# Kernel tuning notes

Hardware: AMD Instinct MI355X
Metric: run time of the kernel (lower is better)

The kernel has to match this reference:

```python
import jax, jax.numpy as jnp
import numpy as np

T, B, I, H, L = 512, 256, 128, 256, 2

def _gru_layer(x, W_ih, W_hh, b_ih, b_hh):
    # x: [T, B, in], W_ih: [3H, in], W_hh: [3H, H], biases: [3H]
    # PyTorch gate order: r, z, n
    Hd = W_hh.shape[1]
    gi = jnp.einsum('tbi,gi->tbg', x, W_ih) + b_ih  # precompute input gates [T,B,3H]

    def step(h, gi_t):
        gh = h @ W_hh.T + b_hh
        i_r, i_z, i_n = jnp.split(gi_t, 3, axis=-1)
        h_r, h_z, h_n = jnp.split(gh, 3, axis=-1)
        r = jax.nn.sigmoid(i_r + h_r)
        z = jax.nn.sigmoid(i_z + h_z)
        n = jnp.tanh(i_n + r * h_n)
        h_new = (1.0 - z) * n + z * h
        return h_new, h_new

    h0 = jnp.zeros((x.shape[1], Hd), dtype=x.dtype)
    _, hs = jax.lax.scan(step, h0, gi)
    return hs  # [T, B, H]

def setup_inputs() -> dict:
    key = jax.random.key(0)
    ks = jax.random.split(key, 11)
    s = 1.0 / np.sqrt(H)
    u = lambda k, shp: jax.random.uniform(k, shp, jnp.float32, -s, s)
    return {
        'x': jax.random.normal(ks[0], (T, B, I), jnp.float32),
        'W_ih0': u(ks[1], (3 * H, I)),
        'W_hh0': u(ks[2], (3 * H, H)),
        'b_ih0': u(ks[3], (3 * H,)),
        'b_hh0': u(ks[4], (3 * H,)),
        'W_ih1': u(ks[5], (3 * H, H)),
        'W_hh1': u(ks[6], (3 * H, H)),
        'b_ih1': u(ks[7], (3 * H,)),
        'b_hh1': u(ks[8], (3 * H,)),
        'W_fc': u(ks[9], (H, H)),
        'b_fc': u(ks[10], (H,)),
    }

def reference(x, W_ih0, W_hh0, b_ih0, b_hh0, W_ih1, W_hh1, b_ih1, b_hh1, W_fc, b_fc):
    h1 = _gru_layer(x, W_ih0, W_hh0, b_ih0, b_hh0)   # [T,B,H]
    h2 = _gru_layer(h1, W_ih1, W_hh1, b_ih1, b_hh1)  # [T,B,H]
    last = h2[-1]                                    # [B,H] last timestep
    return last @ W_fc.T + b_fc
```

## Files before the change

kernel.cpp:

```cpp
#include <hip/hip_runtime.h>

#define TT 512
#define BB 256
#define II 128
#define HH 256
#define LDH 264

typedef __attribute__((ext_vector_type(8))) short short8;
typedef __attribute__((ext_vector_type(4))) float floatx4;
typedef __attribute__((ext_vector_type(4))) float fvec4;
typedef unsigned long long u64;

#define OFF_WIH0 0
#define OFF_WHH0 (OFF_WIH0 + 3 * HH * II)
#define OFF_WIH1 (OFF_WHH0 + 3 * HH * HH)
#define OFF_WHH1 (OFF_WIH1 + 3 * HH * HH)
#define W_TOTAL (OFF_WHH1 + 3 * HH * HH)
#define H1G_OFF W_TOTAL
#define H2G_OFF (H1G_OFF + 2 * BB * HH)
#define WS_SHORTS (H2G_OFF + 2 * BB * HH)
#define FLAGS_OFF_BYTES (WS_SHORTS * 2)
#define FLAG_STRIDE 32

__device__ __forceinline__ short f2bf(float f) {
  unsigned u = __builtin_bit_cast(unsigned, f);
  u = u + 0x7fffu + ((u >> 16) & 1u);
  return (short)(u >> 16);
}
__device__ __forceinline__ float fast_sigmoid(float x) {
  return __fdividef(1.0f, 1.0f + __expf(-x));
}
__device__ __forceinline__ float fast_tanh(float x) {
  return 1.0f - __fdividef(2.0f, 1.0f + __expf(2.0f * x));
}
__device__ __forceinline__ short8 cvt8(const float* __restrict__ p) {
  fvec4 lo = *(const fvec4*)p;
  fvec4 hi = *(const fvec4*)(p + 4);
  short8 r;
  r[0] = f2bf(lo[0]); r[1] = f2bf(lo[1]); r[2] = f2bf(lo[2]); r[3] = f2bf(lo[3]);
  r[4] = f2bf(hi[0]); r[5] = f2bf(hi[1]); r[6] = f2bf(hi[2]); r[7] = f2bf(hi[3]);
  return r;
}
__device__ __forceinline__ u64 ld_sc1(const u64* p) {
  return __hip_atomic_load(p, __ATOMIC_RELAXED, __HIP_MEMORY_SCOPE_AGENT);
}
__device__ __forceinline__ unsigned ld_flag(const unsigned* p) {
  return __hip_atomic_load(p, __ATOMIC_RELAXED, __HIP_MEMORY_SCOPE_AGENT);
}
__device__ __forceinline__ void st_flag(unsigned* p, unsigned v) {
  __hip_atomic_store(p, v, __ATOMIC_RELAXED, __HIP_MEMORY_SCOPE_AGENT);
}

__global__ __launch_bounds__(256) void cvt_weights(
    const float* __restrict__ w0, const float* __restrict__ w1,
    const float* __restrict__ w2, const float* __restrict__ w3,
    short* __restrict__ out) {
  int i = blockIdx.x * 256 + threadIdx.x;
  if (i >= W_TOTAL) return;
  float v;
  if (i < OFF_WHH0)      v = w0[i - OFF_WIH0];
  else if (i < OFF_WIH1) v = w1[i - OFF_WHH0];
  else if (i < OFF_WHH1) v = w2[i - OFF_WIH1];
  else                   v = w3[i - OFF_WHH1];
  out[i] = f2bf(v);
}

__global__ __launch_bounds__(256) void init_state(unsigned* __restrict__ hz,
                                                  unsigned* __restrict__ flags) {
  int i = blockIdx.x * 256 + threadIdx.x;
  if (i < 2 * BB * HH) hz[i] = 0u;
  if (i < 16 * FLAG_STRIDE) flags[i] = 0u;
}

__global__ __launch_bounds__(384) void gru_sync(
    const float* __restrict__ x, const short* __restrict__ wb,
    const float* __restrict__ bih0, const float* __restrict__ bhh0,
    const float* __restrict__ bih1, const float* __restrict__ bhh1,
    const float* __restrict__ Wfc, const float* __restrict__ bfc,
    short* __restrict__ h1g, short* __restrict__ h2g,
    unsigned* __restrict__ flags, float* __restrict__ out) {
  const int tid = threadIdx.x;
  const int lane = tid & 63;
  const int w = tid >> 6;
  const int quad = lane >> 4;
  const int col = lane & 15;
  const int bt = blockIdx.x & 15;
  const int ht = blockIdx.x >> 4;
  const int layer = w / 3, gate = w % 3;
  const int j = ht * 16 + col;

  __shared__ __align__(16) short ldsA[2][16][LDH];
  __shared__ __align__(16) float gt[2][6][16][20];

  const short* wih = wb + (layer ? OFF_WIH1 : OFF_WIH0);
  const short* whh = wb + (layer ? OFF_WHH1 : OFF_WHH0);
  short8 wfI[8], wfH[8];
  if (layer == 0) {
#pragma unroll
    for (int f = 0; f < 4; ++f)
      wfI[f] = *(const short8*)(wih + (gate * HH + j) * II + f * 32 + quad * 8);
#pragma unroll
    for (int f = 4; f < 8; ++f) wfI[f] = short8{0, 0, 0, 0, 0, 0, 0, 0};
  } else {
#pragma unroll
    for (int f = 0; f < 8; ++f)
      wfI[f] = *(const short8*)(wih + (gate * HH + j) * HH + f * 32 + quad * 8);
  }
#pragma unroll
  for (int f = 0; f < 8; ++f)
    wfH[f] = *(const short8*)(whh + (gate * HH + j) * HH + f * 32 + quad * 8);

  const float* bihL = layer ? bih1 : bih0;
  const float* bhhL = layer ? bhh1 : bhh0;
  float bI, bH;
  if (gate == 2) { bI = bihL[2 * HH + j]; bH = bhhL[2 * HH + j]; }
  else { bI = bihL[gate * HH + j] + bhhL[gate * HH + j]; bH = 0.f; }

  float h1a = 0.f, h1b = 0.f, h2a = 0.f, h2b = 0.f;
  const int r1 = tid >> 3, c1 = (tid & 7) * 2;
  const int r2 = (tid - 256) >> 3, c2 = ((tid - 256) & 7) * 2;

  unsigned* fl = flags + bt * FLAG_STRIDE;
  const size_t tbase = (size_t)(bt * 16) * HH;

  for (int p = 0; p <= TT; ++p) {
    short8 ax[4];
    if (w < 3 && p < TT) {
      const float* xr = x + ((size_t)p * BB + bt * 16 + col) * II + quad * 8;
#pragma unroll
      for (int f = 0; f < 4; ++f) ax[f] = cvt8(xr + f * 32);
    }

    if (p > 0) {
      if (tid < 64) {
        const unsigned tgt = (unsigned)p;
        int guard = 0;
        for (;;) {
          unsigned v = tgt;
          if (lane < 16) v = ld_flag(fl + lane);
          if (__all(v >= tgt) || ++guard > (1 << 20)) break;
        }
      }
      __syncthreads();
    }

    {
      const u64* s1 = (const u64*)(h1g + ((p + 1) & 1) * BB * HH + tbase);
      const u64* s2 = (const u64*)(h2g + (p & 1) * BB * HH + tbase);
      u64 t1[4], t2[4];
      if (tid < 256) {
#pragma unroll
        for (int qq = 0; qq < 4; ++qq) t1[qq] = ld_sc1(s1 + tid * 4 + qq);
      }
      if (tid >= 128) {
        const int ti = tid - 128;
#pragma unroll
        for (int qq = 0; qq < 4; ++qq) t2[qq] = ld_sc1(s2 + ti * 4 + qq);
      }
      u64* d1 = (u64*)&ldsA[0][0][0];
      u64* d2 = (u64*)&ldsA[1][0][0];
      if (tid < 256) {
#pragma unroll
        for (int qq = 0; qq < 4; ++qq) {
          int i = tid * 4 + qq, row = i >> 6, c = i & 63;
          d1[row * (LDH / 4) + c] = t1[qq];
        }
      }
      if (tid >= 128) {
        const int ti = tid - 128;
#pragma unroll
        for (int qq = 0; qq < 4; ++qq) {
          int i = ti * 4 + qq, row = i >> 6, c = i & 63;
          d2[row * (LDH / 4) + c] = t2[qq];
        }
      }
    }
    __syncthreads();

    floatx4 aI = floatx4{bI, bI, bI, bI};
    floatx4 aH = floatx4{bH, bH, bH, bH};
    const short* a1 = &ldsA[0][col][0];
    const short* a2 = &ldsA[1][col][0];
    if (layer == 0) {
      if (p < TT) {
#pragma unroll
        for (int f = 0; f < 4; ++f)
          aI = __builtin_amdgcn_mfma_f32_16x16x32_bf16(ax[f], wfI[f], aI, 0, 0, 0);
      }
#pragma unroll
      for (int f = 0; f < 8; ++f) {
        short8 a = *(const short8*)(a1 + f * 32 + quad * 8);
        aH = __builtin_amdgcn_mfma_f32_16x16x32_bf16(a, wfH[f], aH, 0, 0, 0);
      }
    } else {
#pragma unroll
      for (int f = 0; f < 8; ++f) {
        short8 a = *(const short8*)(a1 + f * 32 + quad * 8);
        aI = __builtin_amdgcn_mfma_f32_16x16x32_bf16(a, wfI[f], aI, 0, 0, 0);
      }
#pragma unroll
      for (int f = 0; f < 8; ++f) {
        short8 a = *(const short8*)(a2 + f * 32 + quad * 8);
        aH = __builtin_amdgcn_mfma_f32_16x16x32_bf16(a, wfH[f], aH, 0, 0, 0);
      }
    }
#pragma unroll
    for (int i = 0; i < 4; ++i) {
      gt[0][w][quad * 4 + i][col] = aI[i];
      gt[1][w][quad * 4 + i][col] = aH[i];
    }
    __syncthreads();

    if (tid < 128 && p < TT) {
      float rA = fast_sigmoid(gt[0][0][r1][c1] + gt[1][0][r1][c1]);
      float zA = fast_sigmoid(gt[0][1][r1][c1] + gt[1][1][r1][c1]);
      float nA = fast_tanh(gt[0][2][r1][c1] + rA * gt[1][2][r1][c1]);
      h1a = nA + zA * (h1a - nA);
      float rB = fast_sigmoid(gt[0][0][r1][c1 + 1] + gt[1][0][r1][c1 + 1]);
      float zB = fast_sigmoid(gt[0][1][r1][c1 + 1] + gt[1][1][r1][c1 + 1]);
      float nB = fast_tanh(gt[0][2][r1][c1 + 1] + rB * gt[1][2][r1][c1 + 1]);
      h1b = nB + zB * (h1b - nB);
      unsigned val = ((unsigned)(unsigned short)f2bf(h1b) << 16) |
                     (unsigned)(unsigned short)f2bf(h1a);
      unsigned* dst = (unsigned*)(h1g + (p & 1) * BB * HH +
                                  (bt * 16 + r1) * HH + ht * 16 + c1);
      __hip_atomic_store(dst, val, __ATOMIC_RELAXED, __HIP_MEMORY_SCOPE_AGENT);
    }
    if (tid >= 256 && p > 0) {
      float rA = fast_sigmoid(gt[0][3][r2][c2] + gt[1][3][r2][c2]);
      float zA = fast_sigmoid(gt[0][4][r2][c2] + gt[1][4][r2][c2]);
      float nA = fast_tanh(gt[0][5][r2][c2] + rA * gt[1][5][r2][c2]);
      h2a = nA + zA * (h2a - nA);
      float rB = fast_sigmoid(gt[0][3][r2][c2 + 1] + gt[1][3][r2][c2 + 1]);
      float zB = fast_sigmoid(gt[0][4][r2][c2 + 1] + gt[1][4][r2][c2 + 1]);
      float nB = fast_tanh(gt[0][5][r2][c2 + 1] + rB * gt[1][5][r2][c2 + 1]);
      h2b = nB + zB * (h2b - nB);
      unsigned val = ((unsigned)(unsigned short)f2bf(h2b) << 16) |
                     (unsigned)(unsigned short)f2bf(h2a);
      unsigned* dst = (unsigned*)(h2g + ((p + 1) & 1) * BB * HH +
                                  (bt * 16 + r2) * HH + ht * 16 + c2);
      __hip_atomic_store(dst, val, __ATOMIC_RELAXED, __HIP_MEMORY_SCOPE_AGENT);
    }
    __syncthreads();
    if (tid == 0) st_flag(fl + ht, (unsigned)(p + 1));
  }

  if (tid < 64) {
    const unsigned tgt = (unsigned)(TT + 1);
    int guard = 0;
    for (;;) {
      unsigned v = tgt;
      if (lane < 16) v = ld_flag(fl + lane);
      if (__all(v >= tgt) || ++guard > (1 << 20)) break;
    }
  }
  __syncthreads();
  {
    const u64* s1 = (const u64*)(h2g + 1 * BB * HH + tbase);
    u64 t1[4];
    if (tid < 256) {
#pragma unroll
      for (int qq = 0; qq < 4; ++qq) t1[qq] = ld_sc1(s1 + tid * 4 + qq);
    }
    u64* d1 = (u64*)&ldsA[0][0][0];
    if (tid < 256) {
#pragma unroll
      for (int qq = 0; qq < 4; ++qq) {
        int i = tid * 4 + qq, row = i >> 6, c = i & 63;
        d1[row * (LDH / 4) + c] = t1[qq];
      }
    }
  }
  __syncthreads();
  if (w == 0) {
    float bbv = bfc[j];
    floatx4 acc = floatx4{bbv, bbv, bbv, bbv};
#pragma unroll
    for (int f = 0; f < 8; ++f) {
      short8 a = *(const short8*)(&ldsA[0][col][0] + f * 32 + quad * 8);
      short8 bfrag = cvt8(Wfc + j * HH + f * 32 + quad * 8);
      acc = __builtin_amdgcn_mfma_f32_16x16x32_bf16(a, bfrag, acc, 0, 0, 0);
    }
#pragma unroll
    for (int i = 0; i < 4; ++i)
      out[(size_t)(bt * 16 + quad * 4 + i) * HH + j] = acc[i];
  }
}

extern "C" void kernel_launch(void* const* d_in, const int* in_sizes, int n_in,
                              void* d_out, int out_size, void* d_ws,
                              size_t ws_size, hipStream_t stream) {
  const float* x = (const float*)d_in[0];
  const float* Wih0 = (const float*)d_in[1];
  const float* Whh0 = (const float*)d_in[2];
  const float* bih0 = (const float*)d_in[3];
  const float* bhh0 = (const float*)d_in[4];
  const float* Wih1 = (const float*)d_in[5];
  const float* Whh1 = (const float*)d_in[6];
  const float* bih1 = (const float*)d_in[7];
  const float* bhh1 = (const float*)d_in[8];
  const float* Wfc = (const float*)d_in[9];
  const float* bfc = (const float*)d_in[10];

  short* wb = (short*)d_ws;
  short* h1g = wb + H1G_OFF;
  short* h2g = wb + H2G_OFF;
  unsigned* flags = (unsigned*)((char*)d_ws + FLAGS_OFF_BYTES);
  unsigned* hz = (unsigned*)(wb + H1G_OFF);

  cvt_weights<<<(W_TOTAL + 255) / 256, 256, 0, stream>>>(Wih0, Whh0, Wih1, Whh1, wb);
  init_state<<<(2 * BB * HH + 255) / 256, 256, 0, stream>>>(hz, flags);
  gru_sync<<<256, 384, 0, stream>>>(x, wb, bih0, bhh0, bih1, bhh1, Wfc, bfc,
                                    h1g, h2g, flags, (float*)d_out);
}
```

Baseline: 1.758 ms.

## Interleave four batch groups per block to hide inter-block flag latency

```diff
diff --git a/kernel.cpp b/kernel.cpp
--- a/kernel.cpp
+++ b/kernel.cpp
@@ -84,13 +84,13 @@
   const int w = tid >> 6;
   const int quad = lane >> 4;
   const int col = lane & 15;
-  const int bt = blockIdx.x & 15;
-  const int ht = blockIdx.x >> 4;
+  const int q = blockIdx.x & 3;
+  const int ht = blockIdx.x >> 2;
   const int layer = w / 3, gate = w % 3;
   const int j = ht * 16 + col;
 
-  __shared__ __align__(16) short ldsA[2][16][LDH];
-  __shared__ __align__(16) float gt[2][6][16][20];
+  __shared__ __align__(16) short ldsA[4][2][16][LDH];
+  __shared__ __align__(16) float gt[4][2][6][16][20];
 
   const short* wih = wb + (layer ? OFF_WIH1 : OFF_WIH0);
   const short* whh = wb + (layer ? OFF_WHH1 : OFF_WHH0);
@@ -116,23 +116,21 @@
   if (gate == 2) { bI = bihL[2 * HH + j]; bH = bhhL[2 * HH + j]; }
   else { bI = bihL[gate * HH + j] + bhhL[gate * HH + j]; bH = 0.f; }
 
-  float h1a = 0.f, h1b = 0.f, h2a = 0.f, h2b = 0.f;
   const int r1 = tid >> 3, c1 = (tid & 7) * 2;
   const int r2 = (tid - 256) >> 3, c2 = ((tid - 256) & 7) * 2;
 
-  unsigned* fl = flags + bt * FLAG_STRIDE;
-  const size_t tbase = (size_t)(bt * 16) * HH;
-
-  for (int p = 0; p <= TT; ++p) {
-    short8 ax[4];
-    if (w < 3 && p < TT) {
-      const float* xr = x + ((size_t)p * BB + bt * 16 + col) * II + quad * 8;
-#pragma unroll
-      for (int f = 0; f < 4; ++f) ax[f] = cvt8(xr + f * 32);
-    }
+  float h1aA = 0.f, h1bA = 0.f, h2aA = 0.f, h2bA = 0.f;
+  float h1aB = 0.f, h1bB = 0.f, h2aB = 0.f, h2bB = 0.f;
+  float h1aC = 0.f, h1bC = 0.f, h2aC = 0.f, h2bC = 0.f;
+  float h1aD = 0.f, h1bD = 0.f, h2aD = 0.f, h2bD = 0.f;
+
+  auto slot = [&](int g, int p, short8 (&ax)[4], float& h1a, float& h1b,
+                  float& h2a, float& h2b) {
+    unsigned* fl = flags + (q + 4 * g) * FLAG_STRIDE;
+    const size_t tbase = (size_t)((q + 4 * g) * 16) * HH;
 
     if (p > 0) {
-      if (tid < 64) {
+      if (w == 3) {
         const unsigned tgt = (unsigned)p;
         int guard = 0;
         for (;;) {
@@ -157,8 +155,8 @@
 #pragma unroll
         for (int qq = 0; qq < 4; ++qq) t2[qq] = ld_sc1(s2 + ti * 4 + qq);
       }
-      u64* d1 = (u64*)&ldsA[0][0][0];
-      u64* d2 = (u64*)&ldsA[1][0][0];
+      u64* d1 = (u64*)&ldsA[g][0][0][0];
+      u64* d2 = (u64*)&ldsA[g][1][0][0];
       if (tid < 256) {
 #pragma unroll
         for (int qq = 0; qq < 4; ++qq) {
@@ -179,8 +177,8 @@
 
     floatx4 aI = floatx4{bI, bI, bI, bI};
     floatx4 aH = floatx4{bH, bH, bH, bH};
-    const short* a1 = &ldsA[0][col][0];
-    const short* a2 = &ldsA[1][col][0];
+    const short* a1 = &ldsA[g][0][col][0];
+    const short* a2 = &ldsA[g][1][col][0];
     if (layer == 0) {
       if (p < TT) {
 #pragma unroll
@@ -206,64 +204,81 @@
     }
 #pragma unroll
     for (int i = 0; i < 4; ++i) {
-      gt[0][w][quad * 4 + i][col] = aI[i];
-      gt[1][w][quad * 4 + i][col] = aH[i];
+      gt[g][0][w][quad * 4 + i][col] = aI[i];
+      gt[g][1][w][quad * 4 + i][col] = aH[i];
     }
     __syncthreads();
 
     if (tid < 128 && p < TT) {
-      float rA = fast_sigmoid(gt[0][0][r1][c1] + gt[1][0][r1][c1]);
-      float zA = fast_sigmoid(gt[0][1][r1][c1] + gt[1][1][r1][c1]);
-      float nA = fast_tanh(gt[0][2][r1][c1] + rA * gt[1][2][r1][c1]);
+      float rA = fast_sigmoid(gt[g][0][0][r1][c1] + gt[g][1][0][r1][c1]);
+      float zA = fast_sigmoid(gt[g][0][1][r1][c1] + gt[g][1][1][r1][c1]);
+      float nA = fast_tanh(gt[g][0][2][r1][c1] + rA * gt[g][1][2][r1][c1]);
       h1a = nA + zA * (h1a - nA);
-      float rB = fast_sigmoid(gt[0][0][r1][c1 + 1] + gt[1][0][r1][c1 + 1]);
-      float zB = fast_sigmoid(gt[0][1][r1][c1 + 1] + gt[1][1][r1][c1 + 1]);
-      float nB = fast_tanh(gt[0][2][r1][c1 + 1] + rB * gt[1][2][r1][c1 + 1]);
+      float rB = fast_sigmoid(gt[g][0][0][r1][c1 + 1] + gt[g][1][0][r1][c1 + 1]);
+      float zB = fast_sigmoid(gt[g][0][1][r1][c1 + 1] + gt[g][1][1][r1][c1 + 1]);
+      float nB = fast_tanh(gt[g][0][2][r1][c1 + 1] + rB * gt[g][1][2][r1][c1 + 1]);
       h1b = nB + zB * (h1b - nB);
       unsigned val = ((unsigned)(unsigned short)f2bf(h1b) << 16) |
                      (unsigned)(unsigned short)f2bf(h1a);
       unsigned* dst = (unsigned*)(h1g + (p & 1) * BB * HH +
-                                  (bt * 16 + r1) * HH + ht * 16 + c1);
+                                  ((q + 4 * g) * 16 + r1) * HH + ht * 16 + c1);
       __hip_atomic_store(dst, val, __ATOMIC_RELAXED, __HIP_MEMORY_SCOPE_AGENT);
     }
     if (tid >= 256 && p > 0) {
-      float rA = fast_sigmoid(gt[0][3][r2][c2] + gt[1][3][r2][c2]);
-      float zA = fast_sigmoid(gt[0][4][r2][c2] + gt[1][4][r2][c2]);
-      float nA = fast_tanh(gt[0][5][r2][c2] + rA * gt[1][5][r2][c2]);
+      float rA = fast_sigmoid(gt[g][0][3][r2][c2] + gt[g][1][3][r2][c2]);
+      float zA = fast_sigmoid(gt[g][0][4][r2][c2] + gt[g][1][4][r2][c2]);
+      float nA = fast_tanh(gt[g][0][5][r2][c2] + rA * gt[g][1][5][r2][c2]);
       h2a = nA + zA * (h2a - nA);
-      float rB = fast_sigmoid(gt[0][3][r2][c2 + 1] + gt[1][3][r2][c2 + 1]);
-      float zB = fast_sigmoid(gt[0][4][r2][c2 + 1] + gt[1][4][r2][c2 + 1]);
-      float nB = fast_tanh(gt[0][5][r2][c2 + 1] + rB * gt[1][5][r2][c2 + 1]);
+      float rB = fast_sigmoid(gt[g][0][3][r2][c2 + 1] + gt[g][1][3][r2][c2 + 1]);
+      float zB = fast_sigmoid(gt[g][0][4][r2][c2 + 1] + gt[g][1][4][r2][c2 + 1]);
+      float nB = fast_tanh(gt[g][0][5][r2][c2 + 1] + rB * gt[g][1][5][r2][c2 + 1]);
       h2b = nB + zB * (h2b - nB);
       unsigned val = ((unsigned)(unsigned short)f2bf(h2b) << 16) |
                      (unsigned)(unsigned short)f2bf(h2a);
       unsigned* dst = (unsigned*)(h2g + ((p + 1) & 1) * BB * HH +
-                                  (bt * 16 + r2) * HH + ht * 16 + c2);
+                                  ((q + 4 * g) * 16 + r2) * HH + ht * 16 + c2);
       __hip_atomic_store(dst, val, __ATOMIC_RELAXED, __HIP_MEMORY_SCOPE_AGENT);
     }
     __syncthreads();
     if (tid == 0) st_flag(fl + ht, (unsigned)(p + 1));
-  }
-
-  if (tid < 64) {
+  };
+
+  for (int p = 0; p <= TT; ++p) {
+    short8 axA[4], axB[4], axC[4], axD[4];
+    if (w < 3 && p < TT) {
+      const float* xr = x + ((size_t)p * BB + q * 16 + col) * II + quad * 8;
+#pragma unroll
+      for (int f = 0; f < 4; ++f) {
+        axA[f] = cvt8(xr + f * 32);
+        axB[f] = cvt8(xr + 64 * II + f * 32);
+        axC[f] = cvt8(xr + 128 * II + f * 32);
+        axD[f] = cvt8(xr + 192 * II + f * 32);
+      }
+    }
+    slot(0, p, axA, h1aA, h1bA, h2aA, h2bA);
+    slot(1, p, axB, h1aB, h1bB, h2aB, h2bB);
+    slot(2, p, axC, h1aC, h1bC, h2aC, h2bC);
+    slot(3, p, axD, h1aD, h1bD, h2aD, h2bD);
+  }
+
+  if (w == 3) {
     const unsigned tgt = (unsigned)(TT + 1);
     int guard = 0;
     for (;;) {
-      unsigned v = tgt;
-      if (lane < 16) v = ld_flag(fl + lane);
+      unsigned v = ld_flag(flags + (q + 4 * (lane >> 4)) * FLAG_STRIDE + (lane & 15));
       if (__all(v >= tgt) || ++guard > (1 << 20)) break;
     }
   }
   __syncthreads();
-  {
-    const u64* s1 = (const u64*)(h2g + 1 * BB * HH + tbase);
-    u64 t1[4];
-    if (tid < 256) {
+  if (tid < 256) {
+#pragma unroll
+    for (int g = 0; g < 4; ++g) {
+      const size_t tb = (size_t)((q + 4 * g) * 16) * HH;
+      const u64* s1 = (const u64*)(h2g + 1 * BB * HH + tb);
+      u64 t1[4];
 #pragma unroll
       for (int qq = 0; qq < 4; ++qq) t1[qq] = ld_sc1(s1 + tid * 4 + qq);
-    }
-    u64* d1 = (u64*)&ldsA[0][0][0];
-    if (tid < 256) {
+      u64* d1 = (u64*)&ldsA[g][0][0][0];
 #pragma unroll
       for (int qq = 0; qq < 4; ++qq) {
         int i = tid * 4 + qq, row = i >> 6, c = i & 63;
@@ -272,18 +287,19 @@
     }
   }
   __syncthreads();
-  if (w == 0) {
+  if (w < 4) {
+    const int g = w;
     float bbv = bfc[j];
     floatx4 acc = floatx4{bbv, bbv, bbv, bbv};
 #pragma unroll
     for (int f = 0; f < 8; ++f) {
-      short8 a = *(const short8*)(&ldsA[0][col][0] + f * 32 + quad * 8);
+      short8 a = *(const short8*)(&ldsA[g][0][col][0] + f * 32 + quad * 8);
       short8 bfrag = cvt8(Wfc + j * HH + f * 32 + quad * 8);
       acc = __builtin_amdgcn_mfma_f32_16x16x32_bf16(a, bfrag, acc, 0, 0, 0);
     }
 #pragma unroll
     for (int i = 0; i < 4; ++i)
-      out[(size_t)(bt * 16 + quad * 4 + i) * HH + j] = acc[i];
+      out[(size_t)((q + 4 * g) * 16 + quad * 4 + i) * HH + j] = acc[i];
   }
 }
 
@@ -310,6 +326,6 @@
 
   cvt_weights<<<(W_TOTAL + 255) / 256, 256, 0, stream>>>(Wih0, Whh0, Wih1, Whh1, wb);
   init_state<<<(2 * BB * HH + 255) / 256, 256, 0, stream>>>(hz, flags);
-  gru_sync<<<256, 384, 0, stream>>>(x, wb, bih0, bhh0, bih1, bhh1, Wfc, bfc,
-                                    h1g, h2g, flags, (float*)d_out);
-}
+  gru_sync<<<64, 384, 0, stream>>>(x, wb, bih0, bhh0, bih1, bhh1, Wfc, bfc,
+                                   h1g, h2g, flags, (float*)d_out);
+}
```

After: 6.339 ms. 261% more time.

## Replace flag barriers with step-tagged hidden-state words for per-element synchronization

Applied to the files above, without the earlier changes.

```diff
diff --git a/kernel.cpp b/kernel.cpp
--- a/kernel.cpp
+++ b/kernel.cpp
@@ -16,11 +16,10 @@
 #define OFF_WIH1 (OFF_WHH0 + 3 * HH * HH)
 #define OFF_WHH1 (OFF_WIH1 + 3 * HH * HH)
 #define W_TOTAL (OFF_WHH1 + 3 * HH * HH)
-#define H1G_OFF W_TOTAL
-#define H2G_OFF (H1G_OFF + 2 * BB * HH)
-#define WS_SHORTS (H2G_OFF + 2 * BB * HH)
-#define FLAGS_OFF_BYTES (WS_SHORTS * 2)
-#define FLAG_STRIDE 32
+#define HPAR (BB * (HH / 2))
+#define HT_WORDS (2 * HPAR)
+#define H1T_OFF_BYTES (W_TOTAL * 2)
+#define H2T_OFF_BYTES (H1T_OFF_BYTES + HT_WORDS * 8)
 
 __device__ __forceinline__ short f2bf(float f) {
   unsigned u = __builtin_bit_cast(unsigned, f);
@@ -44,10 +43,7 @@
 __device__ __forceinline__ u64 ld_sc1(const u64* p) {
   return __hip_atomic_load(p, __ATOMIC_RELAXED, __HIP_MEMORY_SCOPE_AGENT);
 }
-__device__ __forceinline__ unsigned ld_flag(const unsigned* p) {
-  return __hip_atomic_load(p, __ATOMIC_RELAXED, __HIP_MEMORY_SCOPE_AGENT);
-}
-__device__ __forceinline__ void st_flag(unsigned* p, unsigned v) {
+__device__ __forceinline__ void st_sc1(u64* p, u64 v) {
   __hip_atomic_store(p, v, __ATOMIC_RELAXED, __HIP_MEMORY_SCOPE_AGENT);
 }
 
@@ -65,11 +61,13 @@
   out[i] = f2bf(v);
 }
 
-__global__ __launch_bounds__(256) void init_state(unsigned* __restrict__ hz,
-                                                  unsigned* __restrict__ flags) {
+__global__ __launch_bounds__(256) void init_state(u64* __restrict__ h1t,
+                                                  u64* __restrict__ h2t) {
   int i = blockIdx.x * 256 + threadIdx.x;
-  if (i < 2 * BB * HH) hz[i] = 0u;
-  if (i < 16 * FLAG_STRIDE) flags[i] = 0u;
+  if (i < HT_WORDS) {
+    h1t[i] = 0ull;
+    h2t[i] = (1ull << 32);
+  }
 }
 
 __global__ __launch_bounds__(384) void gru_sync(
@@ -77,8 +75,7 @@
     const float* __restrict__ bih0, const float* __restrict__ bhh0,
     const float* __restrict__ bih1, const float* __restrict__ bhh1,
     const float* __restrict__ Wfc, const float* __restrict__ bfc,
-    short* __restrict__ h1g, short* __restrict__ h2g,
-    unsigned* __restrict__ flags, float* __restrict__ out) {
+    u64* __restrict__ h1t, u64* __restrict__ h2t, float* __restrict__ out) {
   const int tid = threadIdx.x;
   const int lane = tid & 63;
   const int w = tid >> 6;
@@ -88,6 +85,7 @@
   const int ht = blockIdx.x >> 4;
   const int layer = w / 3, gate = w % 3;
   const int j = ht * 16 + col;
+  (void)lane;
 
   __shared__ __align__(16) short ldsA[2][16][LDH];
   __shared__ __align__(16) float gt[2][6][16][20];
@@ -118,10 +116,10 @@
 
   float h1a = 0.f, h1b = 0.f, h2a = 0.f, h2b = 0.f;
   const int r1 = tid >> 3, c1 = (tid & 7) * 2;
-  const int r2 = (tid - 256) >> 3, c2 = ((tid - 256) & 7) * 2;
-
-  unsigned* fl = flags + bt * FLAG_STRIDE;
-  const size_t tbase = (size_t)(bt * 16) * HH;
+  const int r2 = (tid - 256) >> 3;
+  const int c2 = ((tid - 256) & 7) * 2;
+
+  const int tilebase = bt * 16 * (HH / 2);
 
   for (int p = 0; p <= TT; ++p) {
     short8 ax[4];
@@ -131,47 +129,48 @@
       for (int f = 0; f < 4; ++f) ax[f] = cvt8(xr + f * 32);
     }
 
-    if (p > 0) {
-      if (tid < 64) {
-        const unsigned tgt = (unsigned)p;
-        int guard = 0;
-        for (;;) {
-          unsigned v = tgt;
-          if (lane < 16) v = ld_flag(fl + lane);
-          if (__all(v >= tgt) || ++guard > (1 << 20)) break;
+    u64 w1[8], w2[8];
+    {
+      const u64* s1w = h1t + ((p + 1) & 1) * HPAR + tilebase;
+      const u64* s2w = h2t + (p & 1) * HPAR + tilebase;
+      const unsigned tg = (unsigned)p;
+      int guard = 0;
+      for (;;) {
+        bool ok = true;
+        if (tid < 256) {
+#pragma unroll
+          for (int k = 0; k < 8; ++k) w1[k] = ld_sc1(s1w + tid * 8 + k);
+#pragma unroll
+          for (int k = 0; k < 8; ++k) ok &= ((unsigned)(w1[k] >> 32) == tg);
         }
-      }
-      __syncthreads();
-    }
-
+        if (tid >= 128) {
+          const int ti = tid - 128;
+#pragma unroll
+          for (int k = 0; k < 8; ++k) w2[k] = ld_sc1(s2w + ti * 8 + k);
+#pragma unroll
+          for (int k = 0; k < 8; ++k) ok &= ((unsigned)(w2[k] >> 32) == tg);
+        }
+        if (p == 0 || __all(ok) || ++guard > (1 << 16)) break;
+      }
+    }
     {
-      const u64* s1 = (const u64*)(h1g + ((p + 1) & 1) * BB * HH + tbase);
-      const u64* s2 = (const u64*)(h2g + (p & 1) * BB * HH + tbase);
-      u64 t1[4], t2[4];
-      if (tid < 256) {
-#pragma unroll
-        for (int qq = 0; qq < 4; ++qq) t1[qq] = ld_sc1(s1 + tid * 4 + qq);
-      }
-      if (tid >= 128) {
-        const int ti = tid - 128;
-#pragma unroll
-        for (int qq = 0; qq < 4; ++qq) t2[qq] = ld_sc1(s2 + ti * 4 + qq);
-      }
       u64* d1 = (u64*)&ldsA[0][0][0];
       u64* d2 = (u64*)&ldsA[1][0][0];
       if (tid < 256) {
 #pragma unroll
         for (int qq = 0; qq < 4; ++qq) {
+          u64 v = (w1[2 * qq] & 0xffffffffull) | (w1[2 * qq + 1] << 32);
           int i = tid * 4 + qq, row = i >> 6, c = i & 63;
-          d1[row * (LDH / 4) + c] = t1[qq];
+          d1[row * (LDH / 4) + c] = v;
         }
       }
       if (tid >= 128) {
         const int ti = tid - 128;
 #pragma unroll
         for (int qq = 0; qq < 4; ++qq) {
+          u64 v = (w2[2 * qq] & 0xffffffffull) | (w2[2 * qq + 1] << 32);
           int i = ti * 4 + qq, row = i >> 6, c = i & 63;
-          d2[row * (LDH / 4) + c] = t2[qq];
+          d2[row * (LDH / 4) + c] = v;
         }
       }
     }
@@ -222,9 +221,9 @@
       h1b = nB + zB * (h1b - nB);
       unsigned val = ((unsigned)(unsigned short)f2bf(h1b) << 16) |
                      (unsigned)(unsigned short)f2bf(h1a);
-      unsigned* dst = (unsigned*)(h1g + (p & 1) * BB * HH +
-                                  (bt * 16 + r1) * HH + ht * 16 + c1);
-      __hip_atomic_store(dst, val, __ATOMIC_RELAXED, __HIP_MEMORY_SCOPE_AGENT);
+      u64 pk = (u64)val | ((u64)(unsigned)(p + 1) << 32);
+      u64* dst = h1t + (p & 1) * HPAR + (bt * 16 + r1) * (HH / 2) + ht * 8 + (tid & 7);
+      st_sc1(dst, pk);
     }
     if (tid >= 256 && p > 0) {
       float rA = fast_sigmoid(gt[0][3][r2][c2] + gt[1][3][r2][c2]);
@@ -237,37 +236,35 @@
       h2b = nB + zB * (h2b - nB);
       unsigned val = ((unsigned)(unsigned short)f2bf(h2b) << 16) |
                      (unsigned)(unsigned short)f2bf(h2a);
-      unsigned* dst = (unsigned*)(h2g + ((p + 1) & 1) * BB * HH +
-                                  (bt * 16 + r2) * HH + ht * 16 + c2);
-      __hip_atomic_store(dst, val, __ATOMIC_RELAXED, __HIP_MEMORY_SCOPE_AGENT);
-    }
-    __syncthreads();
-    if (tid == 0) st_flag(fl + ht, (unsigned)(p + 1));
-  }
-
-  if (tid < 64) {
-    const unsigned tgt = (unsigned)(TT + 1);
+      u64 pk = (u64)val | ((u64)(unsigned)(p + 1) << 32);
+      u64* dst = h2t + ((p + 1) & 1) * HPAR + (bt * 16 + r2) * (HH / 2) + ht * 8 +
+                 ((tid - 256) & 7);
+      st_sc1(dst, pk);
+    }
+  }
+
+  {
+    const u64* sw = h2t + 1 * HPAR + tilebase;
+    u64 wf[8];
+    const unsigned tg = (unsigned)(TT + 1);
     int guard = 0;
     for (;;) {
-      unsigned v = tgt;
-      if (lane < 16) v = ld_flag(fl + lane);
-      if (__all(v >= tgt) || ++guard > (1 << 20)) break;
-    }
-  }
-  __syncthreads();
-  {
-    const u64* s1 = (const u64*)(h2g + 1 * BB * HH + tbase);
-    u64 t1[4];
-    if (tid < 256) {
-#pragma unroll
-      for (int qq = 0; qq < 4; ++qq) t1[qq] = ld_sc1(s1 + tid * 4 + qq);
+      bool ok = true;
+      if (tid < 256) {
+#pragma unroll
+        for (int k = 0; k < 8; ++k) wf[k] = ld_sc1(sw + tid * 8 + k);
+#pragma unroll
+        for (int k = 0; k < 8; ++k) ok &= ((unsigned)(wf[k] >> 32) == tg);
+      }
+      if (__all(ok) || ++guard > (1 << 16)) break;
     }
     u64* d1 = (u64*)&ldsA[0][0][0];
     if (tid < 256) {
 #pragma unroll
       for (int qq = 0; qq < 4; ++qq) {
+        u64 v = (wf[2 * qq] & 0xffffffffull) | (wf[2 * qq + 1] << 32);
         int i = tid * 4 + qq, row = i >> 6, c = i & 63;
-        d1[row * (LDH / 4) + c] = t1[qq];
+        d1[row * (LDH / 4) + c] = v;
       }
     }
   }
@@ -303,13 +300,11 @@
   const float* bfc = (const float*)d_in[10];
 
   short* wb = (short*)d_ws;
-  short* h1g = wb + H1G_OFF;
-  short* h2g = wb + H2G_OFF;
-  unsigned* flags = (unsigned*)((char*)d_ws + FLAGS_OFF_BYTES);
-  unsigned* hz = (unsigned*)(wb + H1G_OFF);
+  u64* h1t = (u64*)((char*)d_ws + H1T_OFF_BYTES);
+  u64* h2t = (u64*)((char*)d_ws + H2T_OFF_BYTES);
 
   cvt_weights<<<(W_TOTAL + 255) / 256, 256, 0, stream>>>(Wih0, Whh0, Wih1, Whh1, wb);
-  init_state<<<(2 * BB * HH + 255) / 256, 256, 0, stream>>>(hz, flags);
+  init_state<<<(HT_WORDS + 255) / 256, 256, 0, stream>>>(h1t, h2t);
   gru_sync<<<256, 384, 0, stream>>>(x, wb, bih0, bhh0, bih1, bhh1, Wfc, bfc,
-                                    h1g, h2g, flags, (float*)d_out);
-}
+                                    h1t, h2t, (float*)d_out);
+}
```

After: 2.921 ms. 66.2% more time.

## Widen each block to 32 hidden columns, halving grid and sync participants

Applied to the files above, without the earlier changes.

```diff
diff --git a/kernel.cpp b/kernel.cpp
--- a/kernel.cpp
+++ b/kernel.cpp
@@ -85,40 +85,44 @@
   const int quad = lane >> 4;
   const int col = lane & 15;
   const int bt = blockIdx.x & 15;
-  const int ht = blockIdx.x >> 4;
+  const int sub = blockIdx.x >> 4;
   const int layer = w / 3, gate = w % 3;
-  const int j = ht * 16 + col;
+  const int j0 = sub * 32 + col;
+  const int j1 = j0 + 16;
 
   __shared__ __align__(16) short ldsA[2][16][LDH];
-  __shared__ __align__(16) float gt[2][6][16][20];
+  __shared__ __align__(16) float gt[2][6][16][36];
 
   const short* wih = wb + (layer ? OFF_WIH1 : OFF_WIH0);
   const short* whh = wb + (layer ? OFF_WHH1 : OFF_WHH0);
-  short8 wfI[8], wfH[8];
-  if (layer == 0) {
-#pragma unroll
-    for (int f = 0; f < 4; ++f)
-      wfI[f] = *(const short8*)(wih + (gate * HH + j) * II + f * 32 + quad * 8);
-#pragma unroll
-    for (int f = 4; f < 8; ++f) wfI[f] = short8{0, 0, 0, 0, 0, 0, 0, 0};
-  } else {
-#pragma unroll
-    for (int f = 0; f < 8; ++f)
-      wfI[f] = *(const short8*)(wih + (gate * HH + j) * HH + f * 32 + quad * 8);
-  }
-#pragma unroll
-  for (int f = 0; f < 8; ++f)
-    wfH[f] = *(const short8*)(whh + (gate * HH + j) * HH + f * 32 + quad * 8);
-
+  const int KI = layer ? HH : II;
+  short8 wfI0[8], wfI1[8], wfH0[8], wfH1[8];
+#pragma unroll
+  for (int f = 0; f < 8; ++f) {
+    if (f * 32 < KI) {
+      wfI0[f] = *(const short8*)(wih + (gate * HH + j0) * KI + f * 32 + quad * 8);
+      wfI1[f] = *(const short8*)(wih + (gate * HH + j1) * KI + f * 32 + quad * 8);
+    } else {
+      wfI0[f] = short8{0, 0, 0, 0, 0, 0, 0, 0};
+      wfI1[f] = short8{0, 0, 0, 0, 0, 0, 0, 0};
+    }
+    wfH0[f] = *(const short8*)(whh + (gate * HH + j0) * HH + f * 32 + quad * 8);
+    wfH1[f] = *(const short8*)(whh + (gate * HH + j1) * HH + f * 32 + quad * 8);
+  }
   const float* bihL = layer ? bih1 : bih0;
   const float* bhhL = layer ? bhh1 : bhh0;
-  float bI, bH;
-  if (gate == 2) { bI = bihL[2 * HH + j]; bH = bhhL[2 * HH + j]; }
-  else { bI = bihL[gate * HH + j] + bhhL[gate * HH + j]; bH = 0.f; }
+  float bI_0, bH_0, bI_1, bH_1;
+  if (gate == 2) {
+    bI_0 = bihL[2 * HH + j0]; bH_0 = bhhL[2 * HH + j0];
+    bI_1 = bihL[2 * HH + j1]; bH_1 = bhhL[2 * HH + j1];
+  } else {
+    bI_0 = bihL[gate * HH + j0] + bhhL[gate * HH + j0]; bH_0 = 0.f;
+    bI_1 = bihL[gate * HH + j1] + bhhL[gate * HH + j1]; bH_1 = 0.f;
+  }
 
   float h1a = 0.f, h1b = 0.f, h2a = 0.f, h2b = 0.f;
-  const int r1 = tid >> 3, c1 = (tid & 7) * 2;
-  const int r2 = (tid - 256) >> 3, c2 = ((tid - 256) & 7) * 2;
+  const int r1 = tid >> 4, c1 = (tid & 15) * 2;
+  const int r2 = (tid - 128) >> 4, c2 = ((tid - 128) & 15) * 2;
 
   unsigned* fl = flags + bt * FLAG_STRIDE;
   const size_t tbase = (size_t)(bt * 16) * HH;
@@ -132,12 +136,11 @@
     }
 
     if (p > 0) {
-      if (tid < 64) {
+      if (w == 3) {
         const unsigned tgt = (unsigned)p;
         int guard = 0;
         for (;;) {
-          unsigned v = tgt;
-          if (lane < 16) v = ld_flag(fl + lane);
+          unsigned v = (lane < 8) ? ld_flag(fl + lane) : tgt;
           if (__all(v >= tgt) || ++guard > (1 << 20)) break;
         }
       }
@@ -177,41 +180,50 @@
     }
     __syncthreads();
 
-    floatx4 aI = floatx4{bI, bI, bI, bI};
-    floatx4 aH = floatx4{bH, bH, bH, bH};
+    floatx4 aI0 = floatx4{bI_0, bI_0, bI_0, bI_0};
+    floatx4 aH0 = floatx4{bH_0, bH_0, bH_0, bH_0};
+    floatx4 aI1 = floatx4{bI_1, bI_1, bI_1, bI_1};
+    floatx4 aH1 = floatx4{bH_1, bH_1, bH_1, bH_1};
     const short* a1 = &ldsA[0][col][0];
     const short* a2 = &ldsA[1][col][0];
     if (layer == 0) {
       if (p < TT) {
 #pragma unroll
-        for (int f = 0; f < 4; ++f)
-          aI = __builtin_amdgcn_mfma_f32_16x16x32_bf16(ax[f], wfI[f], aI, 0, 0, 0);
+        for (int f = 0; f < 4; ++f) {
+          aI0 = __builtin_amdgcn_mfma_f32_16x16x32_bf16(ax[f], wfI0[f], aI0, 0, 0, 0);
+          aI1 = __builtin_amdgcn_mfma_f32_16x16x32_bf16(ax[f], wfI1[f], aI1, 0, 0, 0);
+        }
       }
 #pragma unroll
       for (int f = 0; f < 8; ++f) {
         short8 a = *(const short8*)(a1 + f * 32 + quad * 8);
-        aH = __builtin_amdgcn_mfma_f32_16x16x32_bf16(a, wfH[f], aH, 0, 0, 0);
+        aH0 = __builtin_amdgcn_mfma_f32_16x16x32_bf16(a, wfH0[f], aH0, 0, 0, 0);
+        aH1 = __builtin_amdgcn_mfma_f32_16x16x32_bf16(a, wfH1[f], aH1, 0, 0, 0);
       }
     } else {
 #pragma unroll
       for (int f = 0; f < 8; ++f) {
         short8 a = *(const short8*)(a1 + f * 32 + quad * 8);
-        aI = __builtin_amdgcn_mfma_f32_16x16x32_bf16(a, wfI[f], aI, 0, 0, 0);
+        aI0 = __builtin_amdgcn_mfma_f32_16x16x32_bf16(a, wfI0[f], aI0, 0, 0, 0);
+        aI1 = __builtin_amdgcn_mfma_f32_16x16x32_bf16(a, wfI1[f], aI1, 0, 0, 0);
       }
 #pragma unroll
       for (int f = 0; f < 8; ++f) {
         short8 a = *(const short8*)(a2 + f * 32 + quad * 8);
-        aH = __builtin_amdgcn_mfma_f32_16x16x32_bf16(a, wfH[f], aH, 0, 0, 0);
+        aH0 = __builtin_amdgcn_mfma_f32_16x16x32_bf16(a, wfH0[f], aH0, 0, 0, 0);
+        aH1 = __builtin_amdgcn_mfma_f32_16x16x32_bf16(a, wfH1[f], aH1, 0, 0, 0);
       }
     }
 #pragma unroll
     for (int i = 0; i < 4; ++i) {
-      gt[0][w][quad * 4 + i][col] = aI[i];
-      gt[1][w][quad * 4 + i][col] = aH[i];
+      gt[0][w][quad * 4 + i][col] = aI0[i];
+      gt[0][w][quad * 4 + i][col + 16] = aI1[i];
+      gt[1][w][quad * 4 + i][col] = aH0[i];
+      gt[1][w][quad * 4 + i][col + 16] = aH1[i];
     }
     __syncthreads();
 
-    if (tid < 128 && p < TT) {
+    if (tid < 256 && p < TT) {
       float rA = fast_sigmoid(gt[0][0][r1][c1] + gt[1][0][r1][c1]);
       float zA = fast_sigmoid(gt[0][1][r1][c1] + gt[1][1][r1][c1]);
       float nA = fast_tanh(gt[0][2][r1][c1] + rA * gt[1][2][r1][c1]);
@@ -223,10 +235,10 @@
       unsigned val = ((unsigned)(unsigned short)f2bf(h1b) << 16) |
                      (unsigned)(unsigned short)f2bf(h1a);
       unsigned* dst = (unsigned*)(h1g + (p & 1) * BB * HH +
-                                  (bt * 16 + r1) * HH + ht * 16 + c1);
+                                  (bt * 16 + r1) * HH + sub * 32 + c1);
       __hip_atomic_store(dst, val, __ATOMIC_RELAXED, __HIP_MEMORY_SCOPE_AGENT);
     }
-    if (tid >= 256 && p > 0) {
+    if (tid >= 128 && p > 0) {
       float rA = fast_sigmoid(gt[0][3][r2][c2] + gt[1][3][r2][c2]);
       float zA = fast_sigmoid(gt[0][4][r2][c2] + gt[1][4][r2][c2]);
       float nA = fast_tanh(gt[0][5][r2][c2] + rA * gt[1][5][r2][c2]);
@@ -238,19 +250,18 @@
       unsigned val = ((unsigned)(unsigned short)f2bf(h2b) << 16) |
                      (unsigned)(unsigned short)f2bf(h2a);
       unsigned* dst = (unsigned*)(h2g + ((p + 1) & 1) * BB * HH +
-                                  (bt * 16 + r2) * HH + ht * 16 + c2);
+                                  (bt * 16 + r2) * HH + sub * 32 + c2);
       __hip_atomic_store(dst, val, __ATOMIC_RELAXED, __HIP_MEMORY_SCOPE_AGENT);
     }
     __syncthreads();
-    if (tid == 0) st_flag(fl + ht, (unsigned)(p + 1));
-  }
-
-  if (tid < 64) {
+    if (tid == 0) st_flag(fl + sub, (unsigned)(p + 1));
+  }
+
+  if (w == 3) {
     const unsigned tgt = (unsigned)(TT + 1);
     int guard = 0;
     for (;;) {
-      unsigned v = tgt;
-      if (lane < 16) v = ld_flag(fl + lane);
+      unsigned v = (lane < 8) ? ld_flag(fl + lane) : tgt;
       if (__all(v >= tgt) || ++guard > (1 << 20)) break;
     }
   }
@@ -272,18 +283,19 @@
     }
   }
   __syncthreads();
-  if (w == 0) {
-    float bbv = bfc[j];
+  if (w < 2) {
+    const int jf = sub * 32 + w * 16 + col;
+    float bbv = bfc[jf];
     floatx4 acc = floatx4{bbv, bbv, bbv, bbv};
 #pragma unroll
     for (int f = 0; f < 8; ++f) {
       short8 a = *(const short8*)(&ldsA[0][col][0] + f * 32 + quad * 8);
-      short8 bfrag = cvt8(Wfc + j * HH + f * 32 + quad * 8);
+      short8 bfrag = cvt8(Wfc + jf * HH + f * 32 + quad * 8);
       acc = __builtin_amdgcn_mfma_f32_16x16x32_bf16(a, bfrag, acc, 0, 0, 0);
     }
 #pragma unroll
     for (int i = 0; i < 4; ++i)
-      out[(size_t)(bt * 16 + quad * 4 + i) * HH + j] = acc[i];
+      out[(size_t)(bt * 16 + quad * 4 + i) * HH + jf] = acc[i];
   }
 }
 
@@ -310,6 +322,6 @@
 
   cvt_weights<<<(W_TOTAL + 255) / 256, 256, 0, stream>>>(Wih0, Whh0, Wih1, Whh1, wb);
   init_state<<<(2 * BB * HH + 255) / 256, 256, 0, stream>>>(hz, flags);
-  gru_sync<<<256, 384, 0, stream>>>(x, wb, bih0, bhh0, bih1, bhh1, Wfc, bfc,
+  gru_sync<<<128, 384, 0, stream>>>(x, wb, bih0, bhh0, bih1, bhh1, Wfc, bfc,
                                     h1g, h2g, flags, (float*)d_out);
 }
```

Result: slower. 1.996 ms (+13.5%).
